# Performance work log

Measured on AMD Instinct MI355X. Metric: run time of the kernel, lower is better.

The kernel has to match this reference:

```python
import jax, jax.numpy as jnp
import numpy as np

BLOCK = 128


def setup_inputs() -> dict:
    key = jax.random.key(0)
    k_x, k_w, k_s, k_b = jax.random.split(key, 4)
    B, S, IN, OUT = 2, 2048, 4096, 4096
    x = jax.random.normal(k_x, (B, S, IN), dtype=jnp.float32)
    # fp8-quantized weight values (simulate e4m3 rounding, keep fp32 storage)
    w = jax.random.normal(k_w, (OUT, IN), dtype=jnp.float32) * 0.02
    weight = w.astype(jnp.float8_e4m3fn).astype(jnp.float32)
    # per-128x128-block inverse scales
    weight_scale_inv = jax.random.uniform(
        k_s, (OUT // BLOCK, IN // BLOCK), dtype=jnp.float32, minval=0.5, maxval=1.5)
    bias = jax.random.normal(k_b, (OUT,), dtype=jnp.float32) * 0.01
    return {"x": x, "weight": weight, "weight_scale_inv": weight_scale_inv, "bias": bias}


def _dequant(weight, scale_inv):
    # weight: [O, I], scale_inv: [O/128, I/128] -> broadcast each scale over a 128x128 block
    O, I = weight.shape
    w = weight.reshape(O // BLOCK, BLOCK, I // BLOCK, BLOCK)
    w = w * scale_inv[:, None, :, None]
    return w.reshape(O, I)


def reference(x, weight, weight_scale_inv, bias):
    w_deq = _dequant(weight, weight_scale_inv)          # [O, I]
    out = jnp.einsum('bsi,oi->bso', x, w_deq)           # [B, S, O]
    return out + bias
```

## Files before the change

kernel.cpp:

```cpp
#include <hip/hip_runtime.h>
#include <hip/hip_bf16.h>
#include <stdint.h>

typedef __attribute__((ext_vector_type(4))) float f32x4;
typedef __attribute__((ext_vector_type(8))) short short8;

__device__ __forceinline__ ushort f2b(float f) {
    union { __hip_bfloat16 h; ushort u; } c;
    c.h = __float2bfloat16(f);
    return c.u;
}

__device__ __forceinline__ void gload_lds16(const void* g, void* lds) {
    __builtin_amdgcn_global_load_lds((const __attribute__((address_space(1))) void*)g,
                                     (__attribute__((address_space(3))) void*)lds,
                                     16, 0, 0);
}

#define BARRIER()  asm volatile("s_barrier" ::: "memory")
#define VMCNT6()   asm volatile("s_waitcnt vmcnt(6)" ::: "memory")
#define VMCNT8()   asm volatile("s_waitcnt vmcnt(8)" ::: "memory")

__global__ void conv_both_kernel(const float* __restrict__ x, ushort* __restrict__ xb, long n8x,
                                 const float* __restrict__ w, const float* __restrict__ sinv,
                                 ushort* __restrict__ wb, int K, int nbk, long n8w) {
    long i = (long)blockIdx.x * blockDim.x + threadIdx.x;
    if (blockIdx.y == 0) {
        if (i >= n8x) return;
        const float4* xv = (const float4*)x;
        float4 v0 = xv[i * 2], v1 = xv[i * 2 + 1];
        short8 r;
        r[0] = (short)f2b(v0.x); r[1] = (short)f2b(v0.y); r[2] = (short)f2b(v0.z); r[3] = (short)f2b(v0.w);
        r[4] = (short)f2b(v1.x); r[5] = (short)f2b(v1.y); r[6] = (short)f2b(v1.z); r[7] = (short)f2b(v1.w);
        *(short8*)&xb[i * 8] = r;
    } else {
        if (i >= n8w) return;
        long e = i * 8;
        int o, c;
        if (K == 4096) { o = (int)(e >> 12); c = (int)(e & 4095); }
        else { o = (int)(e / K); c = (int)(e - (long)o * K); }
        const float s = sinv[(o >> 7) * nbk + (c >> 7)];
        const float4* wv = (const float4*)(w + e);
        float4 v0 = wv[0], v1 = wv[1];
        short8 r;
        r[0] = (short)f2b(v0.x * s); r[1] = (short)f2b(v0.y * s); r[2] = (short)f2b(v0.z * s); r[3] = (short)f2b(v0.w * s);
        r[4] = (short)f2b(v1.x * s); r[5] = (short)f2b(v1.y * s); r[6] = (short)f2b(v1.z * s); r[7] = (short)f2b(v1.w * s);
        *(short8*)&wb[e] = r;
    }
}

__global__ __launch_bounds__(512, 2)
void gemm256_kernel(const ushort* __restrict__ A, const ushort* __restrict__ Bm,
                    const float* __restrict__ bias, float* __restrict__ C,
                    int M, int N, int K) {
    __shared__ alignas(16) short sm[2][32768];

    const int tid  = threadIdx.x;
    const int lane = tid & 63;
    const int wid  = tid >> 6;
    const int wr   = wid >> 2;
    const int wc   = wid & 3;
    const int nbn  = N >> 8;

    const int nwg = gridDim.x;
    const int swz = (blockIdx.x & 7) * (nwg >> 3) + (blockIdx.x >> 3);
    const int bm  = swz / nbn;
    const int bn  = swz % nbn;

    const short* gA = (const short*)A + (size_t)bm * 256 * K;
    const short* gB = (const short*)Bm + (size_t)bn * 256 * K;

    auto STAGE = [&](const short* gOp, int opOff, int kh, int kt, int buf) {
#pragma unroll
        for (int g = 0; g < 2; ++g) {
            int R = wid * 32 + g * 16 + (lane >> 2);
            int chunk = (lane & 3) ^ ((R >> 1) & 3);
            const short* src = gOp + (size_t)R * K + kt * 64 + kh * 32 + chunk * 8;
            gload_lds16(src, &sm[buf][opOff + kh * 8192 + wid * 1024 + g * 512]);
        }
    };

    auto LD_A = [&](int buf, int kh, int mh, short8 (&a)[4]) {
#pragma unroll
        for (int m = 0; m < 4; ++m) {
            int row = wr * 128 + mh * 64 + m * 16 + (lane & 15);
            a[m] = *(const short8*)&sm[buf][kh * 8192 + row * 32 + ((((lane >> 4) ^ ((row >> 1) & 3))) << 3)];
        }
    };
    auto LD_B = [&](int buf, int kh, short8 (&b)[4]) {
#pragma unroll
        for (int n = 0; n < 4; ++n) {
            int row = wc * 64 + n * 16 + (lane & 15);
            b[n] = *(const short8*)&sm[buf][16384 + kh * 8192 + row * 32 + ((((lane >> 4) ^ ((row >> 1) & 3))) << 3)];
        }
    };

    f32x4 acc[8][4] = {};

    auto MFMA_H = [&](int off, short8 (&af)[4], short8 (&bf)[4], int m0, int m1) {
#pragma unroll
        for (int m = m0; m < m1; ++m)
#pragma unroll
            for (int n = 0; n < 4; ++n)
                acc[off + m][n] = __builtin_amdgcn_mfma_f32_16x16x32_bf16(af[m], bf[n], acc[off + m][n], 0, 0, 0);
    };

    const int nkt = K >> 6;

    short8 aCur[4], bCur[4];

    auto KSTEP = [&](int t) {
        const int b  = t & 1;
        const int nb = b ^ 1;
        const int t1 = (t + 1 < nkt) ? t + 1 : nkt - 1;
        const int t2 = (t + 2 < nkt) ? t + 2 : nkt - 1;

        short8 aB[4], aC[4], aD[4], bB[4];

        BARRIER();
        __builtin_amdgcn_s_setprio(1);
        MFMA_H(0, aCur, bCur, 0, 2);
        LD_A(b, 0, 1, aB);
        MFMA_H(0, aCur, bCur, 2, 4);
        __builtin_amdgcn_s_setprio(0);
        STAGE(gA, 0, 1, t1, nb);
        VMCNT6();

        BARRIER();
        __builtin_amdgcn_s_setprio(1);
        MFMA_H(4, aB, bCur, 0, 2);
        LD_A(b, 1, 0, aC);
        LD_B(b, 1, bB);
        MFMA_H(4, aB, bCur, 2, 4);
        __builtin_amdgcn_s_setprio(0);
        STAGE(gB, 16384, 1, t1, nb);
        VMCNT6();

        BARRIER();
        __builtin_amdgcn_s_setprio(1);
        MFMA_H(0, aC, bB, 0, 2);
        LD_A(b, 1, 1, aD);
        MFMA_H(0, aC, bB, 2, 4);
        __builtin_amdgcn_s_setprio(0);
        STAGE(gA, 0, 0, t2, b);
        VMCNT6();

        BARRIER();
        __builtin_amdgcn_s_setprio(1);
        MFMA_H(4, aD, bB, 0, 2);
        LD_A(nb, 0, 0, aCur);
        LD_B(nb, 0, bCur);
        MFMA_H(4, aD, bB, 2, 4);
        __builtin_amdgcn_s_setprio(0);
        STAGE(gB, 16384, 0, t2, b);
        VMCNT6();
    };

    {
        STAGE(gA, 0, 0, 0, 0);
        STAGE(gB, 16384, 0, 0, 0);
        STAGE(gA, 0, 1, 0, 0);
        STAGE(gB, 16384, 1, 0, 0);
        STAGE(gA, 0, 0, 1, 1);
        STAGE(gB, 16384, 0, 1, 1);
        VMCNT8();
        BARRIER();
        LD_A(0, 0, 0, aCur);
        LD_B(0, 0, bCur);
    }

    for (int t = 0; t < nkt; t += 2) {
        KSTEP(t);
        KSTEP(t + 1);
    }

    const int r0 = bm * 256 + wr * 128 + (lane >> 4) * 4;
    const int c0 = bn * 256 + wc * 64 + (lane & 15);
#pragma unroll
    for (int n = 0; n < 4; ++n) {
        float bv = bias[c0 + n * 16];
#pragma unroll
        for (int m = 0; m < 8; ++m) {
#pragma unroll
            for (int r = 0; r < 4; ++r) {
                C[(size_t)(r0 + m * 16 + r) * N + (c0 + n * 16)] = acc[m][n][r] + bv;
            }
        }
    }
}

__global__ void fallback_gemm(const float* __restrict__ x, const float* __restrict__ w,
                              const float* __restrict__ sinv, const float* __restrict__ bias,
                              float* __restrict__ out, int M, int N, int K) {
    int n = blockIdx.x * 64 + (threadIdx.x & 63);
    int m = blockIdx.y * 4 + (threadIdx.x >> 6);
    if (m >= M || n >= N) return;
    const int nbk = K >> 7;
    float acc = 0.f;
    for (int k = 0; k < K; ++k)
        acc += x[(size_t)m * K + k] * w[(size_t)n * K + k] * sinv[(n >> 7) * nbk + (k >> 7)];
    out[(size_t)m * N + n] = acc + bias[n];
}

extern "C" void kernel_launch(void* const* d_in, const int* in_sizes, int n_in,
                              void* d_out, int out_size, void* d_ws, size_t ws_size,
                              hipStream_t stream) {
    const float* x    = (const float*)d_in[0];
    const float* w    = (const float*)d_in[1];
    const float* sinv = (const float*)d_in[2];
    const float* bias = (const float*)d_in[3];
    float* out        = (float*)d_out;

    const int O = in_sizes[3];
    const int K = in_sizes[1] / O;
    const int M = (int)((long)in_sizes[0] / K);
    const int N = O;

    const size_t need = ((size_t)M * K + (size_t)N * K) * sizeof(ushort);
    const int nwg = (M / 256) * (N / 256);
    const bool ok = ws_size >= need && (M % 256 == 0) && (N % 256 == 0) &&
                    (K % 128 == 0) && (nwg % 8 == 0) && ((long)M * K % 2048 == 0) &&
                    (K % 2048 == 0);
    if (ok) {
        ushort* xb = (ushort*)d_ws;
        ushort* wb = xb + (size_t)M * K;
        long n8x = (long)M * K / 8;
        long n8w = (long)N * K / 8;
        long n8m = (n8x > n8w) ? n8x : n8w;
        dim3 cg((unsigned)((n8m + 255) / 256), 2);
        conv_both_kernel<<<cg, 256, 0, stream>>>(x, xb, n8x, w, sinv, wb, K, K >> 7, n8w);
        gemm256_kernel<<<dim3(nwg), 512, 0, stream>>>(xb, wb, bias, out, M, N, K);
    } else {
        dim3 g(N / 64, (M + 3) / 4);
        fallback_gemm<<<g, 256, 0, stream>>>(x, w, sinv, bias, out, M, N, K);
    }
}
```

Measured before the change: 284.2 us.

## Switch GEMM to 32x32x16 MFMA tiles with two-phase K-step pipeline

Replaces the 16x16x32 bf16 MFMA tiling with 32x32x16 MFMA instructions, so each wave holds 4x2 accumulator tiles of 16 floats. The K-step is restructured from four barrier-separated phases into two, each issuing an A and a B staging load together, with the wait count and LDS fragment loading reorganised to match. The larger MFMA shape should raise math density per LDS read and cut barrier count per K tile. The cost is longer dependency chains per instruction and a different register footprint under the 2-waves-per-SIMD launch bound.

```diff
diff --git a/kernel.cpp b/kernel.cpp
--- a/kernel.cpp
+++ b/kernel.cpp
@@ -2,7 +2,7 @@
 #include <hip/hip_bf16.h>
 #include <stdint.h>
 
-typedef __attribute__((ext_vector_type(4))) float f32x4;
+typedef __attribute__((ext_vector_type(16))) float f32x16;
 typedef __attribute__((ext_vector_type(8))) short short8;
 
 __device__ __forceinline__ ushort f2b(float f) {
@@ -18,8 +18,7 @@
 }
 
 #define BARRIER()  asm volatile("s_barrier" ::: "memory")
-#define VMCNT6()   asm volatile("s_waitcnt vmcnt(6)" ::: "memory")
-#define VMCNT8()   asm volatile("s_waitcnt vmcnt(8)" ::: "memory")
+#define VMCNT4()   asm volatile("s_waitcnt vmcnt(4)" ::: "memory")
 
 __global__ void conv_both_kernel(const float* __restrict__ x, ushort* __restrict__ xb, long n8x,
                                  const float* __restrict__ w, const float* __restrict__ sinv,
@@ -80,34 +79,51 @@
         }
     };
 
-    auto LD_A = [&](int buf, int kh, int mh, short8 (&a)[4]) {
-#pragma unroll
-        for (int m = 0; m < 4; ++m) {
-            int row = wr * 128 + mh * 64 + m * 16 + (lane & 15);
-            a[m] = *(const short8*)&sm[buf][kh * 8192 + row * 32 + ((((lane >> 4) ^ ((row >> 1) & 3))) << 3)];
-        }
-    };
-    auto LD_B = [&](int buf, int kh, short8 (&b)[4]) {
-#pragma unroll
-        for (int n = 0; n < 4; ++n) {
-            int row = wc * 64 + n * 16 + (lane & 15);
-            b[n] = *(const short8*)&sm[buf][16384 + kh * 8192 + row * 32 + ((((lane >> 4) ^ ((row >> 1) & 3))) << 3)];
-        }
-    };
-
-    f32x4 acc[8][4] = {};
-
-    auto MFMA_H = [&](int off, short8 (&af)[4], short8 (&bf)[4], int m0, int m1) {
-#pragma unroll
-        for (int m = m0; m < m1; ++m)
-#pragma unroll
-            for (int n = 0; n < 4; ++n)
-                acc[off + m][n] = __builtin_amdgcn_mfma_f32_16x16x32_bf16(af[m], bf[n], acc[off + m][n], 0, 0, 0);
-    };
+    auto LD_A32 = [&](int buf, int kh, int s, int mt, short8& a) {
+        int row = wr * 128 + mt * 32 + (lane & 31);
+        int chunk = ((s << 1) + (lane >> 5)) ^ ((row >> 1) & 3);
+        a = *(const short8*)&sm[buf][kh * 8192 + row * 32 + (chunk << 3)];
+    };
+    auto LD_B32 = [&](int buf, int kh, int s, int nt, short8& bfr) {
+        int row = wc * 64 + nt * 32 + (lane & 31);
+        int chunk = ((s << 1) + (lane >> 5)) ^ ((row >> 1) & 3);
+        bfr = *(const short8*)&sm[buf][16384 + kh * 8192 + row * 32 + (chunk << 3)];
+    };
+
+    f32x16 acc[4][2] = {};
 
     const int nkt = K >> 6;
 
-    short8 aCur[4], bCur[4];
+    short8 aCur[2][4], bCur[2][2];
+
+    auto PHASE = [&](short8 (&aU)[2][4], short8 (&bU)[2][2],
+                     int fb, int fkh, short8 (&aV)[2][4], short8 (&bV)[2][2]) {
+        __builtin_amdgcn_s_setprio(1);
+#pragma unroll
+        for (int mt = 0; mt < 2; ++mt)
+#pragma unroll
+            for (int nt = 0; nt < 2; ++nt)
+                acc[mt][nt] = __builtin_amdgcn_mfma_f32_32x32x16_bf16(aU[0][mt], bU[0][nt], acc[mt][nt], 0, 0, 0);
+#pragma unroll
+        for (int mt = 0; mt < 4; ++mt) LD_A32(fb, fkh, 0, mt, aV[0][mt]);
+#pragma unroll
+        for (int nt = 0; nt < 2; ++nt) LD_B32(fb, fkh, 0, nt, bV[0][nt]);
+#pragma unroll
+        for (int mt = 2; mt < 4; ++mt)
+#pragma unroll
+            for (int nt = 0; nt < 2; ++nt)
+                acc[mt][nt] = __builtin_amdgcn_mfma_f32_32x32x16_bf16(aU[0][mt], bU[0][nt], acc[mt][nt], 0, 0, 0);
+#pragma unroll
+        for (int mt = 0; mt < 4; ++mt) LD_A32(fb, fkh, 1, mt, aV[1][mt]);
+#pragma unroll
+        for (int nt = 0; nt < 2; ++nt) LD_B32(fb, fkh, 1, nt, bV[1][nt]);
+#pragma unroll
+        for (int mt = 0; mt < 4; ++mt)
+#pragma unroll
+            for (int nt = 0; nt < 2; ++nt)
+                acc[mt][nt] = __builtin_amdgcn_mfma_f32_32x32x16_bf16(aU[1][mt], bU[1][nt], acc[mt][nt], 0, 0, 0);
+        __builtin_amdgcn_s_setprio(0);
+    };
 
     auto KSTEP = [&](int t) {
         const int b  = t & 1;
@@ -115,45 +131,19 @@
         const int t1 = (t + 1 < nkt) ? t + 1 : nkt - 1;
         const int t2 = (t + 2 < nkt) ? t + 2 : nkt - 1;
 
-        short8 aB[4], aC[4], aD[4], bB[4];
+        short8 aN[2][4], bN[2][2];
 
         BARRIER();
-        __builtin_amdgcn_s_setprio(1);
-        MFMA_H(0, aCur, bCur, 0, 2);
-        LD_A(b, 0, 1, aB);
-        MFMA_H(0, aCur, bCur, 2, 4);
-        __builtin_amdgcn_s_setprio(0);
+        PHASE(aCur, bCur, b, 1, aN, bN);
         STAGE(gA, 0, 1, t1, nb);
-        VMCNT6();
+        STAGE(gB, 16384, 1, t1, nb);
+        VMCNT4();
 
         BARRIER();
-        __builtin_amdgcn_s_setprio(1);
-        MFMA_H(4, aB, bCur, 0, 2);
-        LD_A(b, 1, 0, aC);
-        LD_B(b, 1, bB);
-        MFMA_H(4, aB, bCur, 2, 4);
-        __builtin_amdgcn_s_setprio(0);
-        STAGE(gB, 16384, 1, t1, nb);
-        VMCNT6();
-
-        BARRIER();
-        __builtin_amdgcn_s_setprio(1);
-        MFMA_H(0, aC, bB, 0, 2);
-        LD_A(b, 1, 1, aD);
-        MFMA_H(0, aC, bB, 2, 4);
-        __builtin_amdgcn_s_setprio(0);
+        PHASE(aN, bN, nb, 0, aCur, bCur);
         STAGE(gA, 0, 0, t2, b);
-        VMCNT6();
-
-        BARRIER();
-        __builtin_amdgcn_s_setprio(1);
-        MFMA_H(4, aD, bB, 0, 2);
-        LD_A(nb, 0, 0, aCur);
-        LD_B(nb, 0, bCur);
-        MFMA_H(4, aD, bB, 2, 4);
-        __builtin_amdgcn_s_setprio(0);
         STAGE(gB, 16384, 0, t2, b);
-        VMCNT6();
+        VMCNT4();
     };
 
     {
@@ -163,10 +153,15 @@
         STAGE(gB, 16384, 1, 0, 0);
         STAGE(gA, 0, 0, 1, 1);
         STAGE(gB, 16384, 0, 1, 1);
-        VMCNT8();
+        VMCNT4();
         BARRIER();
-        LD_A(0, 0, 0, aCur);
-        LD_B(0, 0, bCur);
+#pragma unroll
+        for (int s = 0; s < 2; ++s) {
+#pragma unroll
+            for (int mt = 0; mt < 4; ++mt) LD_A32(0, 0, s, mt, aCur[s][mt]);
+#pragma unroll
+            for (int nt = 0; nt < 2; ++nt) LD_B32(0, 0, s, nt, bCur[s][nt]);
+        }
     }
 
     for (int t = 0; t < nkt; t += 2) {
@@ -174,16 +169,18 @@
         KSTEP(t + 1);
     }
 
-    const int r0 = bm * 256 + wr * 128 + (lane >> 4) * 4;
-    const int c0 = bn * 256 + wc * 64 + (lane & 15);
-#pragma unroll
-    for (int n = 0; n < 4; ++n) {
-        float bv = bias[c0 + n * 16];
-#pragma unroll
-        for (int m = 0; m < 8; ++m) {
-#pragma unroll
-            for (int r = 0; r < 4; ++r) {
-                C[(size_t)(r0 + m * 16 + r) * N + (c0 + n * 16)] = acc[m][n][r] + bv;
+    const int r0 = bm * 256 + wr * 128;
+    const int c0 = bn * 256 + wc * 64;
+#pragma unroll
+    for (int nt = 0; nt < 2; ++nt) {
+        const int col = c0 + nt * 32 + (lane & 31);
+        float bv = bias[col];
+#pragma unroll
+        for (int mt = 0; mt < 4; ++mt) {
+#pragma unroll
+            for (int r = 0; r < 16; ++r) {
+                int row = r0 + mt * 32 + (r & 3) + 8 * (r >> 2) + 4 * (lane >> 5);
+                C[(size_t)row * N + col] = acc[mt][nt][r] + bv;
             }
         }
     }
```

After: 285.4 us. No clear change (+0.4%).
